# Performance work log

Measured on AMD Instinct MI355X. Metric: run time of the kernel, lower is better.

Reference implementation:

```python
import jax, jax.numpy as jnp
import numpy as np

B = 32768
N_AGENTS, N_CAPS, CAP_DIM, AGENT_DIM = 4, 10, 32, 64


def squash(t, axis=-1):
    sq = jnp.sum(jnp.square(t), axis=axis, keepdims=True)
    scale = sq / (1.0 + sq) / jnp.sqrt(sq + 1e-8)
    return scale * t


def setup_inputs() -> dict:
    key = jax.random.key(0)
    ks = jax.random.split(key, 6)
    # Kaiming-ish small init for linears, randn for routing W (as in torch source)
    x = jax.random.normal(ks[0], (B, 784), dtype=jnp.float32)
    W1 = jax.random.normal(ks[1], (N_AGENTS, 784, AGENT_DIM), dtype=jnp.float32) * (1.0 / np.sqrt(784))
    b1 = jnp.zeros((N_AGENTS, AGENT_DIM), dtype=jnp.float32)
    W2 = jax.random.normal(ks[2], (N_AGENTS, AGENT_DIM, AGENT_DIM), dtype=jnp.float32) * (1.0 / np.sqrt(AGENT_DIM))
    b2 = jnp.zeros((N_AGENTS, AGENT_DIM), dtype=jnp.float32)
    W = jax.random.normal(ks[3], (N_AGENTS, N_CAPS, CAP_DIM, AGENT_DIM), dtype=jnp.float32)
    return {"x": x, "W1": W1, "b1": b1, "W2": W2, "b2": b2, "W": W}


def reference(x, W1, b1, W2, b2, W):
    # --- 4 agents, vectorized over the agent axis 'a' ---
    h = jax.nn.relu(jnp.einsum('bi,aio->bao', x, W1) + b1)          # [B, 4, 64]
    u = squash(jnp.einsum('bah,aho->bao', h, W2) + b2, axis=-1)      # [B, 4, 64]
    # torch: matmul(W[B,4,10,32,64], u[B,4,1,64,1]) -> [B,4,10,32]
    u_hat = jnp.einsum('ajik,bak->baji', W, u)                       # [B, 4, 10, 32]
    # --- dynamic routing, 3 iterations ---
    logits = jnp.zeros((x.shape[0], N_AGENTS, N_CAPS, 1), dtype=u_hat.dtype)
    v = None
    for it in range(3):
        c = jax.nn.softmax(logits, axis=2)                            # over the 10 capsules
        s = jnp.sum(c * u_hat, axis=1, keepdims=True)                 # [B, 1, 10, 32]
        v = squash(s, axis=-1)                                        # [B, 1, 10, 32]
        if it < 2:
            agreement = jnp.sum(u_hat * v, axis=-1, keepdims=True)    # [B, 4, 10, 1]
            logits = logits + agreement
    return jnp.squeeze(v, axis=1)                                     # [B, 10, 32]
```

## Files before the change

### kernel.cpp

```cpp
#include <hip/hip_runtime.h>

typedef __bf16 bf16_t;
typedef bf16_t bf16x8 __attribute__((ext_vector_type(8)));
typedef unsigned short u16x8 __attribute__((ext_vector_type(8)));
typedef float f32x4 __attribute__((ext_vector_type(4)));
typedef unsigned int u32x4 __attribute__((ext_vector_type(4)));

union BF8 { u16x8 u; bf16x8 b; };

__device__ __forceinline__ unsigned short f2bf(float f) {
  unsigned int u = __float_as_uint(f);
  unsigned int r = (u + 0x7FFFu + ((u >> 16) & 1u)) >> 16;
  return (unsigned short)r;
}
__device__ __forceinline__ float bf2f(unsigned short s) {
  return __uint_as_float(((unsigned int)s) << 16);
}

__global__ __launch_bounds__(256) void kprep(const float* __restrict__ W1,
                                             const float* __restrict__ W2,
                                             const float* __restrict__ W,
                                             unsigned short* __restrict__ Wfh,
                                             unsigned short* __restrict__ Wfl,
                                             unsigned short* __restrict__ W2h,
                                             unsigned short* __restrict__ W2l,
                                             unsigned short* __restrict__ Wfb) {
  int idx = blockIdx.x * 256 + threadIdx.x;
  if (idx < 204800) {
    int e = idx & 7, lane = (idx >> 3) & 63, nt = (idx >> 9) & 15, ks = idx >> 13;
    int k = ks * 32 + (lane >> 4) * 8 + e;
    int col = nt * 16 + (lane & 15);
    int a = col >> 6, o = col & 63;
    float v = (k < 784) ? W1[(a * 784 + k) * 64 + o] : 0.f;
    unsigned short hi = f2bf(v);
    Wfh[idx] = hi;
    Wfl[idx] = f2bf(v - bf2f(hi));
  }
  if (idx < 16384) {
    int a = idx >> 12, o = (idx >> 6) & 63, k = idx & 63;
    float v = W2[(a * 64 + k) * 64 + o];
    unsigned short hi = f2bf(v);
    W2h[idx] = hi;
    W2l[idx] = f2bf(v - bf2f(hi));
  }
  if (idx < 81920) {
    int e = idx & 7;
    int t = idx >> 3;
    int lane = t & 63; t >>= 6;
    int kc = t & 1;   t >>= 1;
    int nt = t % 20;
    int a  = t / 20;
    int row = nt * 16 + (lane & 15);
    int kk  = kc * 32 + (lane >> 4) * 8 + e;
    Wfb[idx] = f2bf(W[(a * 320 + row) * 64 + kk]);
  }
}

__global__ __launch_bounds__(512, 4) void kA(const float* __restrict__ x,
                                             const float* __restrict__ b1,
                                             const unsigned short* __restrict__ Wfh,
                                             const unsigned short* __restrict__ Wfl,
                                             unsigned int* __restrict__ H) {
  __shared__ unsigned short xsh[2][64 * 40];
  __shared__ unsigned short xsl[2][64 * 40];
  __shared__ float b1s[256];
  const int tid = threadIdx.x;
  const int w   = tid >> 6;
  const int l   = tid & 63;
  const int l15 = l & 15;
  const int lg4 = l >> 4;
  const int k8  = lg4 * 8;
  const int b0  = blockIdx.x * 64;

  if (tid < 256) b1s[tid] = b1[tid];

  const f32x4 fz = {0.f, 0.f, 0.f, 0.f};
  f32x4 acc[4][2];
#pragma unroll
  for (int mt = 0; mt < 4; ++mt)
#pragma unroll
    for (int n = 0; n < 2; ++n) acc[mt][n] = fz;

  const int srow = tid >> 3;
  const int skq  = (tid & 7) * 4;
  const float* xrow = x + (size_t)(b0 + srow) * 784;

  {
    f32x4 xv = fz;
    if (skq < 784) xv = *(const f32x4*)(xrow + skq);
    unsigned int ph[2], pl[2];
#pragma unroll
    for (int j = 0; j < 2; ++j) {
      unsigned short h0 = f2bf(xv[2 * j]), h1 = f2bf(xv[2 * j + 1]);
      unsigned short s0 = f2bf(xv[2 * j] - bf2f(h0));
      unsigned short s1 = f2bf(xv[2 * j + 1] - bf2f(h1));
      ph[j] = (unsigned int)h0 | ((unsigned int)h1 << 16);
      pl[j] = (unsigned int)s0 | ((unsigned int)s1 << 16);
    }
    *(uint2*)&xsh[0][srow * 40 + skq] = *(uint2*)ph;
    *(uint2*)&xsl[0][srow * 40 + skq] = *(uint2*)pl;
  }

  for (int ks = 0; ks < 25; ++ks) {
    const int cur = ks & 1;
    f32x4 xn = fz;
    if (ks < 24) {
      int kf = (ks + 1) * 32 + skq;
      if (kf < 784) xn = *(const f32x4*)(xrow + kf);
    }
    __syncthreads();

    const int nt0 = w * 2;
    bf16x8 bh0 = *(const bf16x8*)(Wfh + ((size_t)(ks * 16 + nt0) * 64 + l) * 8);
    bf16x8 bl0 = *(const bf16x8*)(Wfl + ((size_t)(ks * 16 + nt0) * 64 + l) * 8);
    bf16x8 bh1 = *(const bf16x8*)(Wfh + ((size_t)(ks * 16 + nt0 + 1) * 64 + l) * 8);
    bf16x8 bl1 = *(const bf16x8*)(Wfl + ((size_t)(ks * 16 + nt0 + 1) * 64 + l) * 8);

    bf16x8 ah[4], al[4];
#pragma unroll
    for (int mt = 0; mt < 4; ++mt) {
      ah[mt] = *(const bf16x8*)&xsh[cur][(mt * 16 + l15) * 40 + k8];
      al[mt] = *(const bf16x8*)&xsl[cur][(mt * 16 + l15) * 40 + k8];
    }

#pragma unroll
    for (int mt = 0; mt < 4; ++mt) {
      acc[mt][0] = __builtin_amdgcn_mfma_f32_16x16x32_bf16(ah[mt], bh0, acc[mt][0], 0, 0, 0);
      acc[mt][0] = __builtin_amdgcn_mfma_f32_16x16x32_bf16(al[mt], bh0, acc[mt][0], 0, 0, 0);
      acc[mt][0] = __builtin_amdgcn_mfma_f32_16x16x32_bf16(ah[mt], bl0, acc[mt][0], 0, 0, 0);
      acc[mt][1] = __builtin_amdgcn_mfma_f32_16x16x32_bf16(ah[mt], bh1, acc[mt][1], 0, 0, 0);
      acc[mt][1] = __builtin_amdgcn_mfma_f32_16x16x32_bf16(al[mt], bh1, acc[mt][1], 0, 0, 0);
      acc[mt][1] = __builtin_amdgcn_mfma_f32_16x16x32_bf16(ah[mt], bl1, acc[mt][1], 0, 0, 0);
    }

    if (ks < 24) {
      unsigned int ph[2], pl[2];
#pragma unroll
      for (int j = 0; j < 2; ++j) {
        unsigned short h0 = f2bf(xn[2 * j]), h1 = f2bf(xn[2 * j + 1]);
        unsigned short s0 = f2bf(xn[2 * j] - bf2f(h0));
        unsigned short s1 = f2bf(xn[2 * j + 1] - bf2f(h1));
        ph[j] = (unsigned int)h0 | ((unsigned int)h1 << 16);
        pl[j] = (unsigned int)s0 | ((unsigned int)s1 << 16);
      }
      *(uint2*)&xsh[cur ^ 1][srow * 40 + skq] = *(uint2*)ph;
      *(uint2*)&xsl[cur ^ 1][srow * 40 + skq] = *(uint2*)pl;
    }
  }

#pragma unroll
  for (int mt = 0; mt < 4; ++mt)
#pragma unroll
    for (int n = 0; n < 2; ++n) {
      int col = (w * 2 + n) * 16 + l15;
      float bb = b1s[col];
#pragma unroll
      for (int r = 0; r < 4; ++r) {
        int row = b0 + mt * 16 + lg4 * 4 + r;
        float v = acc[mt][n][r] + bb;
        v = v > 0.f ? v : 0.f;
        unsigned short hi = f2bf(v);
        unsigned short lo = f2bf(v - bf2f(hi));
        H[(size_t)row * 256 + col] = (unsigned int)hi | ((unsigned int)lo << 16);
      }
    }
}

__global__ __launch_bounds__(256, 3) void kB(const unsigned int* __restrict__ H,
                                             const float* __restrict__ b2,
                                             const unsigned short* __restrict__ W2h,
                                             const unsigned short* __restrict__ W2l,
                                             const unsigned short* __restrict__ Wfb,
                                             float* __restrict__ out) {
  __shared__ float smem[13056];
  const int tid = threadIdx.x;
  const int a   = tid >> 6;
  const int l   = tid & 63;
  const int l15 = l & 15;
  const int lg4 = l >> 4;
  const int k8  = lg4 * 8;
  const int b0  = blockIdx.x * 16;

  bf16x8 hh[2], hl[2];
#pragma unroll
  for (int kc = 0; kc < 2; ++kc) {
    const u32x4* hp = (const u32x4*)(H + (size_t)(b0 + l15) * 256 + a * 64 + kc * 32 + k8);
    u32x4 q0 = __builtin_nontemporal_load(hp);
    u32x4 q1 = __builtin_nontemporal_load(hp + 1);
    unsigned int pw[8] = {q0[0], q0[1], q0[2], q0[3], q1[0], q1[1], q1[2], q1[3]};
    BF8 vh, vl;
#pragma unroll
    for (int j = 0; j < 8; ++j) {
      vh.u[j] = (unsigned short)(pw[j] & 0xFFFFu);
      vl.u[j] = (unsigned short)(pw[j] >> 16);
    }
    hh[kc] = vh.b;
    hl[kc] = vl.b;
  }
  const f32x4 fz = {0.f, 0.f, 0.f, 0.f};
  f32x4 a2[4];
#pragma unroll
  for (int ot = 0; ot < 4; ++ot) a2[ot] = fz;
#pragma unroll
  for (int ot = 0; ot < 4; ++ot)
#pragma unroll
    for (int kc = 0; kc < 2; ++kc) {
      bf16x8 bh = *(const bf16x8*)(W2h + ((a * 64 + ot * 16 + l15) * 64 + kc * 32 + k8));
      bf16x8 bl = *(const bf16x8*)(W2l + ((a * 64 + ot * 16 + l15) * 64 + kc * 32 + k8));
      a2[ot] = __builtin_amdgcn_mfma_f32_16x16x32_bf16(hh[kc], bh, a2[ot], 0, 0, 0);
      a2[ot] = __builtin_amdgcn_mfma_f32_16x16x32_bf16(hl[kc], bh, a2[ot], 0, 0, 0);
      a2[ot] = __builtin_amdgcn_mfma_f32_16x16x32_bf16(hh[kc], bl, a2[ot], 0, 0, 0);
    }
  float b2v[4];
#pragma unroll
  for (int ot = 0; ot < 4; ++ot) b2v[ot] = b2[a * 64 + ot * 16 + l15];
#pragma unroll
  for (int r = 0; r < 4; ++r) {
    float up[4];
    float sq = 0.f;
#pragma unroll
    for (int ot = 0; ot < 4; ++ot) {
      float v = a2[ot][r] + b2v[ot];
      up[ot] = v;
      sq += v * v;
    }
    sq += __shfl_xor(sq, 1, 64);
    sq += __shfl_xor(sq, 2, 64);
    sq += __shfl_xor(sq, 4, 64);
    sq += __shfl_xor(sq, 8, 64);
    float scale = sq / ((1.f + sq) * sqrtf(sq + 1e-8f));
#pragma unroll
    for (int ot = 0; ot < 4; ++ot)
      smem[a * 1088 + (lg4 * 4 + r) * 68 + ot * 16 + l15] = scale * up[ot];
  }
  __syncthreads();

  bf16x8 uah[2], ual[2];
#pragma unroll
  for (int kc = 0; kc < 2; ++kc) {
    float4 f0 = *(const float4*)&smem[a * 1088 + l15 * 68 + kc * 32 + k8];
    float4 f1 = *(const float4*)&smem[a * 1088 + l15 * 68 + kc * 32 + k8 + 4];
    float vv[8] = {f0.x, f0.y, f0.z, f0.w, f1.x, f1.y, f1.z, f1.w};
    BF8 vh, vl;
#pragma unroll
    for (int j = 0; j < 8; ++j) {
      unsigned short hi = f2bf(vv[j]);
      vh.u[j] = hi;
      vl.u[j] = f2bf(vv[j] - bf2f(hi));
    }
    uah[kc] = vh.b;
    ual[kc] = vl.b;
  }
  __syncthreads();

  f32x4 au[20];
#pragma unroll
  for (int nt = 0; nt < 20; ++nt) au[nt] = fz;
#pragma unroll
  for (int nt = 0; nt < 20; ++nt)
#pragma unroll
    for (int kc = 0; kc < 2; ++kc) {
      bf16x8 bh = *(const bf16x8*)(Wfb + ((size_t)((a * 20 + nt) * 2 + kc) * 64 + l) * 8);
      au[nt] = __builtin_amdgcn_mfma_f32_16x16x32_bf16(uah[kc], bh, au[nt], 0, 0, 0);
      au[nt] = __builtin_amdgcn_mfma_f32_16x16x32_bf16(ual[kc], bh, au[nt], 0, 0, 0);
    }

  const int sid   = tid >> 4;
  const int jraw  = tid & 15;
  const bool jact = (jraw < 10);
  const int jj    = jact ? jraw : 9;
  const int rbase = sid * 204 + jj * 20;

  float Gp[10];
#pragma unroll
  for (int p = 0; p < 10; ++p) Gp[p] = 0.f;

#pragma unroll
  for (int hh2 = 0; hh2 < 2; ++hh2) {
    const int half = 1 - hh2;
    if (hh2 > 0) __syncthreads();
#pragma unroll
    for (int q = 0; q < 10; ++q)
#pragma unroll
      for (int r = 0; r < 4; ++r)
        smem[(a * 16 + lg4 * 4 + r) * 204 + q * 20 + l15] = au[q * 2 + half][r];
    __syncthreads();
#pragma unroll
    for (int qq = 0; qq < 4; ++qq) {
      f32x4 f0 = *(const f32x4*)&smem[rbase + 0 * 3264 + qq * 4];
      f32x4 f1 = *(const f32x4*)&smem[rbase + 1 * 3264 + qq * 4];
      f32x4 f2 = *(const f32x4*)&smem[rbase + 2 * 3264 + qq * 4];
      f32x4 f3 = *(const f32x4*)&smem[rbase + 3 * 3264 + qq * 4];
#pragma unroll
      for (int e = 0; e < 4; ++e) {
        float v0 = f0[e], v1 = f1[e], v2 = f2[e], v3 = f3[e];
        Gp[0] += v0 * v0; Gp[1] += v0 * v1; Gp[2] += v0 * v2; Gp[3] += v0 * v3;
        Gp[4] += v1 * v1; Gp[5] += v1 * v2; Gp[6] += v1 * v3;
        Gp[7] += v2 * v2; Gp[8] += v2 * v3;
        Gp[9] += v3 * v3;
      }
    }
  }

  float cf0 = 0.f, cf1 = 0.f, cf2 = 0.f, cf3 = 0.f;
  {
    float lg0 = 0.f, lg1 = 0.f, lg2 = 0.f, lg3 = 0.f;
#pragma unroll
    for (int it = 0; it < 3; ++it) {
      float e0 = jact ? __expf(lg0) : 0.f;
      float e1 = jact ? __expf(lg1) : 0.f;
      float e2 = jact ? __expf(lg2) : 0.f;
      float e3 = jact ? __expf(lg3) : 0.f;
      float S0 = e0, S1 = e1, S2 = e2, S3 = e3;
#pragma unroll
      for (int m = 1; m <= 8; m <<= 1) {
        S0 += __shfl_xor(S0, m, 16);
        S1 += __shfl_xor(S1, m, 16);
        S2 += __shfl_xor(S2, m, 16);
        S3 += __shfl_xor(S3, m, 16);
      }
      float c0 = e0 / S0, c1 = e1 / S1, c2 = e2 / S2, c3 = e3 / S3;
      float t0 = c0 * Gp[0] + c1 * Gp[1] + c2 * Gp[2] + c3 * Gp[3];
      float t1 = c0 * Gp[1] + c1 * Gp[4] + c2 * Gp[5] + c3 * Gp[6];
      float t2 = c0 * Gp[2] + c1 * Gp[5] + c2 * Gp[7] + c3 * Gp[8];
      float t3 = c0 * Gp[3] + c1 * Gp[6] + c2 * Gp[8] + c3 * Gp[9];
      float sq = c0 * t0 + c1 * t1 + c2 * t2 + c3 * t3;
      float scale = sq / ((1.f + sq) * sqrtf(sq + 1e-8f));
      if (it < 2) {
        lg0 += scale * t0;
        lg1 += scale * t1;
        lg2 += scale * t2;
        lg3 += scale * t3;
      } else {
        cf0 = scale * c0;
        cf1 = scale * c1;
        cf2 = scale * c2;
        cf3 = scale * c3;
      }
    }
  }

  float* po = out + (size_t)(b0 + sid) * 320 + jraw * 32;
  if (jact) {
#pragma unroll
    for (int qq = 0; qq < 4; ++qq) {
      f32x4 f0 = *(const f32x4*)&smem[rbase + 0 * 3264 + qq * 4];
      f32x4 f1 = *(const f32x4*)&smem[rbase + 1 * 3264 + qq * 4];
      f32x4 f2 = *(const f32x4*)&smem[rbase + 2 * 3264 + qq * 4];
      f32x4 f3 = *(const f32x4*)&smem[rbase + 3 * 3264 + qq * 4];
      f32x4 v4;
#pragma unroll
      for (int e = 0; e < 4; ++e)
        v4[e] = cf0 * f0[e] + cf1 * f1[e] + cf2 * f2[e] + cf3 * f3[e];
      *(f32x4*)(po + qq * 4) = v4;
    }
  }
  __syncthreads();
#pragma unroll
  for (int q = 0; q < 10; ++q)
#pragma unroll
    for (int r = 0; r < 4; ++r)
      smem[(a * 16 + lg4 * 4 + r) * 204 + q * 20 + l15] = au[q * 2 + 1][r];
  __syncthreads();
  if (jact) {
#pragma unroll
    for (int qq = 0; qq < 4; ++qq) {
      f32x4 f0 = *(const f32x4*)&smem[rbase + 0 * 3264 + qq * 4];
      f32x4 f1 = *(const f32x4*)&smem[rbase + 1 * 3264 + qq * 4];
      f32x4 f2 = *(const f32x4*)&smem[rbase + 2 * 3264 + qq * 4];
      f32x4 f3 = *(const f32x4*)&smem[rbase + 3 * 3264 + qq * 4];
      f32x4 v4;
#pragma unroll
      for (int e = 0; e < 4; ++e)
        v4[e] = cf0 * f0[e] + cf1 * f1[e] + cf2 * f2[e] + cf3 * f3[e];
      *(f32x4*)(po + 16 + qq * 4) = v4;
    }
  }
}

extern "C" void kernel_launch(void* const* d_in, const int* in_sizes, int n_in,
                              void* d_out, int out_size, void* d_ws, size_t ws_size,
                              hipStream_t stream) {
  const float* x  = (const float*)d_in[0];
  const float* W1 = (const float*)d_in[1];
  const float* b1 = (const float*)d_in[2];
  const float* W2 = (const float*)d_in[3];
  const float* b2 = (const float*)d_in[4];
  const float* W  = (const float*)d_in[5];

  unsigned short* wsb = (unsigned short*)d_ws;
  unsigned short* Wfh = wsb;
  unsigned short* Wfl = wsb + 204800;
  unsigned short* W2h = wsb + 409600;
  unsigned short* W2l = wsb + 425984;
  unsigned short* Wfb = wsb + 442368;
  unsigned int*   H   = (unsigned int*)(wsb + 606208);
  float* out = (float*)d_out;

  kprep<<<800, 256, 0, stream>>>(W1, W2, W, Wfh, Wfl, W2h, W2l, Wfb);
  kA<<<512, 512, 0, stream>>>(x, b1, Wfh, Wfl, H);
  kB<<<2048, 256, 0, stream>>>(H, b2, W2h, W2l, Wfb, out);
}
```

Baseline: 102.6 us.

## Split u_hat MFMA by capsule halves, swizzle LDS, recompute first half for output

Kernel kB no longer keeps all 20 u_hat accumulator tiles live. It computes 10 tiles per capsule half, covering 5 capsules across the full 32 dims. Those go to a smaller XOR-swizzled shared-memory layout (160 floats per row) meant to avoid bank conflicts, and the first half is recomputed with extra MFMAs for the final output pass. Fewer live registers and less LDS let launch bounds rise from 3 to 4 blocks per SM. In exchange the kernel does a third batch of MFMAs, and only 5 of the 16 lanes in each group are active per Gram pass.

```diff
diff --git a/kernel.cpp b/kernel.cpp
--- a/kernel.cpp
+++ b/kernel.cpp
@@ -166,13 +166,26 @@
     }
 }
 
-__global__ __launch_bounds__(256, 3) void kB(const unsigned int* __restrict__ H,
+__device__ __forceinline__ void rd4(const float* smem, int sid, int jloc, int iq,
+                                    f32x4& f0, f32x4& f1, f32x4& f2, f32x4& f3) {
+  int r0 = 0 * 16 + sid, s0 = ((r0 ^ jloc) & 7) << 2;
+  int r1 = 1 * 16 + sid, s1 = ((r1 ^ jloc) & 7) << 2;
+  int r2 = 2 * 16 + sid, s2 = ((r2 ^ jloc) & 7) << 2;
+  int r3 = 3 * 16 + sid, s3 = ((r3 ^ jloc) & 7) << 2;
+  int c = jloc * 32 + iq * 4;
+  f0 = *(const f32x4*)&smem[r0 * 160 + (c ^ s0)];
+  f1 = *(const f32x4*)&smem[r1 * 160 + (c ^ s1)];
+  f2 = *(const f32x4*)&smem[r2 * 160 + (c ^ s2)];
+  f3 = *(const f32x4*)&smem[r3 * 160 + (c ^ s3)];
+}
+
+__global__ __launch_bounds__(256, 4) void kB(const unsigned int* __restrict__ H,
                                              const float* __restrict__ b2,
                                              const unsigned short* __restrict__ W2h,
                                              const unsigned short* __restrict__ W2l,
                                              const unsigned short* __restrict__ Wfb,
                                              float* __restrict__ out) {
-  __shared__ float smem[13056];
+  __shared__ float smem[10240];
   const int tid = threadIdx.x;
   const int a   = tid >> 6;
   const int l   = tid & 63;
@@ -253,51 +266,55 @@
   }
   __syncthreads();
 
-  f32x4 au[20];
-#pragma unroll
-  for (int nt = 0; nt < 20; ++nt) au[nt] = fz;
-#pragma unroll
-  for (int nt = 0; nt < 20; ++nt)
-#pragma unroll
-    for (int kc = 0; kc < 2; ++kc) {
-      bf16x8 bh = *(const bf16x8*)(Wfb + ((size_t)((a * 20 + nt) * 2 + kc) * 64 + l) * 8);
-      au[nt] = __builtin_amdgcn_mfma_f32_16x16x32_bf16(uah[kc], bh, au[nt], 0, 0, 0);
-      au[nt] = __builtin_amdgcn_mfma_f32_16x16x32_bf16(ual[kc], bh, au[nt], 0, 0, 0);
-    }
-
-  const int sid   = tid >> 4;
-  const int jraw  = tid & 15;
+  const int sid  = tid >> 4;
+  const int jraw = tid & 15;
   const bool jact = (jraw < 10);
-  const int jj    = jact ? jraw : 9;
-  const int rbase = sid * 204 + jj * 20;
 
   float Gp[10];
 #pragma unroll
   for (int p = 0; p < 10; ++p) Gp[p] = 0.f;
 
-#pragma unroll
-  for (int hh2 = 0; hh2 < 2; ++hh2) {
-    const int half = 1 - hh2;
-    if (hh2 > 0) __syncthreads();
-#pragma unroll
-    for (int q = 0; q < 10; ++q)
-#pragma unroll
-      for (int r = 0; r < 4; ++r)
-        smem[(a * 16 + lg4 * 4 + r) * 204 + q * 20 + l15] = au[q * 2 + half][r];
+  f32x4 au10[10];
+
+#pragma unroll
+  for (int jh = 0; jh < 2; ++jh) {
+#pragma unroll
+    for (int q = 0; q < 10; ++q) {
+      f32x4 acc = fz;
+#pragma unroll
+      for (int kc = 0; kc < 2; ++kc) {
+        bf16x8 bh = *(const bf16x8*)(Wfb + ((size_t)((a * 20 + jh * 10 + q) * 2 + kc) * 64 + l) * 8);
+        acc = __builtin_amdgcn_mfma_f32_16x16x32_bf16(uah[kc], bh, acc, 0, 0, 0);
+        acc = __builtin_amdgcn_mfma_f32_16x16x32_bf16(ual[kc], bh, acc, 0, 0, 0);
+      }
+      au10[q] = acc;
+    }
+    if (jh) __syncthreads();
+#pragma unroll
+    for (int q = 0; q < 10; ++q) {
+      const int cj = q >> 1;
+#pragma unroll
+      for (int r = 0; r < 4; ++r) {
+        int row  = a * 16 + lg4 * 4 + r;
+        int phys = (q * 16 + l15) ^ (((row ^ cj) & 7) << 2);
+        smem[row * 160 + phys] = au10[q][r];
+      }
+    }
     __syncthreads();
-#pragma unroll
-    for (int qq = 0; qq < 4; ++qq) {
-      f32x4 f0 = *(const f32x4*)&smem[rbase + 0 * 3264 + qq * 4];
-      f32x4 f1 = *(const f32x4*)&smem[rbase + 1 * 3264 + qq * 4];
-      f32x4 f2 = *(const f32x4*)&smem[rbase + 2 * 3264 + qq * 4];
-      f32x4 f3 = *(const f32x4*)&smem[rbase + 3 * 3264 + qq * 4];
-#pragma unroll
-      for (int e = 0; e < 4; ++e) {
-        float v0 = f0[e], v1 = f1[e], v2 = f2[e], v3 = f3[e];
-        Gp[0] += v0 * v0; Gp[1] += v0 * v1; Gp[2] += v0 * v2; Gp[3] += v0 * v3;
-        Gp[4] += v1 * v1; Gp[5] += v1 * v2; Gp[6] += v1 * v3;
-        Gp[7] += v2 * v2; Gp[8] += v2 * v3;
-        Gp[9] += v3 * v3;
+    if (jact && jraw >= 5 * jh && jraw < 5 * jh + 5) {
+      const int jloc = jraw - 5 * jh;
+#pragma unroll
+      for (int iq = 0; iq < 8; ++iq) {
+        f32x4 f0, f1, f2, f3;
+        rd4(smem, sid, jloc, iq, f0, f1, f2, f3);
+#pragma unroll
+        for (int e = 0; e < 4; ++e) {
+          float v0 = f0[e], v1 = f1[e], v2 = f2[e], v3 = f3[e];
+          Gp[0] += v0 * v0; Gp[1] += v0 * v1; Gp[2] += v0 * v2; Gp[3] += v0 * v3;
+          Gp[4] += v1 * v1; Gp[5] += v1 * v2; Gp[6] += v1 * v3;
+          Gp[7] += v2 * v2; Gp[8] += v2 * v3;
+          Gp[9] += v3 * v3;
+        }
       }
     }
   }
@@ -341,39 +358,54 @@
   }
 
   float* po = out + (size_t)(b0 + sid) * 320 + jraw * 32;
-  if (jact) {
-#pragma unroll
-    for (int qq = 0; qq < 4; ++qq) {
-      f32x4 f0 = *(const f32x4*)&smem[rbase + 0 * 3264 + qq * 4];
-      f32x4 f1 = *(const f32x4*)&smem[rbase + 1 * 3264 + qq * 4];
-      f32x4 f2 = *(const f32x4*)&smem[rbase + 2 * 3264 + qq * 4];
-      f32x4 f3 = *(const f32x4*)&smem[rbase + 3 * 3264 + qq * 4];
+  if (jact && jraw >= 5) {
+    const int jloc = jraw - 5;
+#pragma unroll
+    for (int iq = 0; iq < 8; ++iq) {
+      f32x4 f0, f1, f2, f3;
+      rd4(smem, sid, jloc, iq, f0, f1, f2, f3);
       f32x4 v4;
 #pragma unroll
       for (int e = 0; e < 4; ++e)
         v4[e] = cf0 * f0[e] + cf1 * f1[e] + cf2 * f2[e] + cf3 * f3[e];
-      *(f32x4*)(po + qq * 4) = v4;
+      *(f32x4*)(po + iq * 4) = v4;
     }
   }
   __syncthreads();
-#pragma unroll
-  for (int q = 0; q < 10; ++q)
-#pragma unroll
-    for (int r = 0; r < 4; ++r)
-      smem[(a * 16 + lg4 * 4 + r) * 204 + q * 20 + l15] = au[q * 2 + 1][r];
+
+#pragma unroll
+  for (int q = 0; q < 10; ++q) {
+    f32x4 acc = fz;
+#pragma unroll
+    for (int kc = 0; kc < 2; ++kc) {
+      bf16x8 bh = *(const bf16x8*)(Wfb + ((size_t)((a * 20 + q) * 2 + kc) * 64 + l) * 8);
+      acc = __builtin_amdgcn_mfma_f32_16x16x32_bf16(uah[kc], bh, acc, 0, 0, 0);
+      acc = __builtin_amdgcn_mfma_f32_16x16x32_bf16(ual[kc], bh, acc, 0, 0, 0);
+    }
+    au10[q] = acc;
+  }
+#pragma unroll
+  for (int q = 0; q < 10; ++q) {
+    const int cj = q >> 1;
+#pragma unroll
+    for (int r = 0; r < 4; ++r) {
+      int row  = a * 16 + lg4 * 4 + r;
+      int phys = (q * 16 + l15) ^ (((row ^ cj) & 7) << 2);
+      smem[row * 160 + phys] = au10[q][r];
+    }
+  }
   __syncthreads();
-  if (jact) {
-#pragma unroll
-    for (int qq = 0; qq < 4; ++qq) {
-      f32x4 f0 = *(const f32x4*)&smem[rbase + 0 * 3264 + qq * 4];
-      f32x4 f1 = *(const f32x4*)&smem[rbase + 1 * 3264 + qq * 4];
-      f32x4 f2 = *(const f32x4*)&smem[rbase + 2 * 3264 + qq * 4];
-      f32x4 f3 = *(const f32x4*)&smem[rbase + 3 * 3264 + qq * 4];
+  if (jact && jraw < 5) {
+    const int jloc = jraw;
+#pragma unroll
+    for (int iq = 0; iq < 8; ++iq) {
+      f32x4 f0, f1, f2, f3;
+      rd4(smem, sid, jloc, iq, f0, f1, f2, f3);
       f32x4 v4;
 #pragma unroll
       for (int e = 0; e < 4; ++e)
         v4[e] = cf0 * f0[e] + cf1 * f1[e] + cf2 * f2[e] + cf3 * f3[e];
-      *(f32x4*)(po + 16 + qq * 4) = v4;
+      *(f32x4*)(po + iq * 4) = v4;
     }
   }
 }
```

Result: slower. 139.1 us (+35.6%).
